# Kernel optimization log

Hardware: AMD Instinct MI355X
Metric: run time of the kernel (lower is better)

The kernel has to match this reference:

```python
import jax, jax.numpy as jnp
import numpy as np

N_HEADS = 16

def _rotate_half(t):
    d = t.shape[-1] // 2
    return jnp.concatenate([-t[..., d:], t[..., :d]], axis=-1)

def _apply_rope(t, cos, sin):
    # t: [B,S,H,dh], cos/sin: [S,1,dh] broadcast over B and H
    return t * cos + _rotate_half(t) * sin

def setup_inputs() -> dict:
    key = jax.random.key(0)
    ks = jax.random.split(key, 7)
    B, S, D = 2, 2048, 2048
    dh = D // N_HEADS
    scale = 1.0 / np.sqrt(D)
    return {
        "x": jax.random.normal(ks[0], (B, S, D), dtype=jnp.float32),
        "rope_cos": jax.random.uniform(ks[1], (S, dh), dtype=jnp.float32),
        "rope_sin": jax.random.uniform(ks[2], (S, dh), dtype=jnp.float32),
        "Wq": jax.random.normal(ks[3], (D, D), dtype=jnp.float32) * scale,
        "Wk": jax.random.normal(ks[4], (D, D), dtype=jnp.float32) * scale,
        "Wv": jax.random.normal(ks[5], (D, D), dtype=jnp.float32) * scale,
        "Wo": jax.random.normal(ks[6], (D, D), dtype=jnp.float32) * scale,
    }

def reference(x, rope_cos, rope_sin, Wq, Wk, Wv, Wo):
    B, S, D = x.shape
    H = N_HEADS
    dh = D // H
    # QKV projections (nn.Linear: x @ W.T), reshape to heads
    q = (x @ Wq.T).reshape(B, S, H, dh)
    k = (x @ Wk.T).reshape(B, S, H, dh)
    v = (x @ Wv.T).reshape(B, S, H, dh)
    cos = rope_cos[:, None, :]  # [S,1,dh]
    sin = rope_sin[:, None, :]
    q = _apply_rope(q, cos, sin)
    k = _apply_rope(k, cos, sin)
    # Attention: [B,H,S,S] scores, scaled softmax
    scores = jnp.einsum("bqhd,bkhd->bhqk", q, k) / jnp.sqrt(jnp.asarray(dh, dtype=x.dtype))
    probs = jax.nn.softmax(scores, axis=-1)
    out = jnp.einsum("bhqk,bkhd->bqhd", probs, v).reshape(B, S, D)
    return out @ Wo.T
```

## Files before the change

kernel.cpp:

```cpp
#include <hip/hip_runtime.h>
#include <hip/hip_bf16.h>

typedef unsigned short u16;
typedef __bf16 bf16x8 __attribute__((ext_vector_type(8)));
typedef float f32x4 __attribute__((ext_vector_type(4)));

__device__ __forceinline__ float bf2f(u16 u) {
  union { unsigned int i; float f; } v; v.i = ((unsigned int)u) << 16; return v.f;
}
__device__ __forceinline__ u16 f2bf(float f) {
  union { float f; unsigned int i; } v; v.f = f;
  unsigned int r = v.i + 0x7fffu + ((v.i >> 16) & 1u);
  return (u16)(r >> 16);
}
__device__ __forceinline__ unsigned cvtpk(float lo, float hi) {
  unsigned r;
  asm("v_cvt_pk_bf16_f32 %0, %1, %2" : "=v"(r) : "v"(lo), "v"(hi));
  return r;
}

__device__ __forceinline__ void async_load16(void* lds, const void* g) {
  __builtin_amdgcn_global_load_lds((const __attribute__((address_space(1))) void*)g,
                                   (__attribute__((address_space(3))) void*)lds, 16, 0, 0);
}

__global__ void convert_all(const float* __restrict__ x, const float* __restrict__ Wq,
                            const float* __restrict__ Wk, const float* __restrict__ Wv,
                            const float* __restrict__ Wo, u16* __restrict__ xb,
                            u16* __restrict__ Wqkb, u16* __restrict__ Wvb,
                            u16* __restrict__ Wob) {
  int bid = blockIdx.x;
  const float* src;
  u16* dst;
  int off;
  if (bid < 8192)       { src = x;  dst = xb;              off = bid; }
  else if (bid < 12288) { src = Wq; dst = Wqkb;            off = bid - 8192; }
  else if (bid < 16384) { src = Wk; dst = Wqkb + 4194304;  off = bid - 12288; }
  else if (bid < 20480) { src = Wv; dst = Wvb;             off = bid - 16384; }
  else                  { src = Wo; dst = Wob;             off = bid - 20480; }
  int i = off * 1024 + threadIdx.x * 4;
  float4 v = *(const float4*)(src + i);
  ushort4 o;
  o.x = f2bf(v.x); o.y = f2bf(v.y); o.z = f2bf(v.z); o.w = f2bf(v.w);
  *(ushort4*)(dst + i) = o;
}

template <int ROPE>
__device__ __forceinline__ void gemm256_body(const u16* __restrict__ A,
                                             const u16* __restrict__ Bm,
                                             u16* __restrict__ C, int M, int N, int K,
                                             int tm, int tn, u16* lds,
                                             const float* __restrict__ cosb,
                                             const float* __restrict__ sinb,
                                             float qscale) {
  const int t = threadIdx.x;
  const int w = t >> 6, l = t & 63;
  const int wm = w >> 2, wn = w & 3;
  const int lr = l & 15, lh = l >> 4;
  const size_t row0 = (size_t)tm * 256, col0 = (size_t)tn * 256;
  const u16* Ag = A + row0 * K;
  const u16* Bg = Bm + col0 * K;

  const int ra = t >> 2, kc = (t & 3) << 3;
  auto stage = [&](int s) {
    u16* dst = lds + (s & 3) * 16384;
    const size_t koff = (size_t)s * 32 + kc;
    async_load16(dst + t * 8,         Ag + (size_t)ra * K + koff);
    async_load16(dst + 4096 + t * 8,  Ag + (size_t)(ra + 128) * K + koff);
    async_load16(dst + 8192 + t * 8,  Bg + (size_t)ra * K + koff);
    async_load16(dst + 12288 + t * 8, Bg + (size_t)(ra + 128) * K + koff);
  };

  f32x4 acc[8][4];
#pragma unroll
  for (int i = 0; i < 8; ++i)
#pragma unroll
    for (int j = 0; j < 4; ++j) acc[i][j] = (f32x4){0.f, 0.f, 0.f, 0.f};

  const int NK = K >> 5;
  stage(0); stage(1); stage(2);

  for (int s = 0; s < NK; ++s) {
    if (s + 2 < NK)      asm volatile("s_waitcnt vmcnt(8)" ::: "memory");
    else if (s + 1 < NK) asm volatile("s_waitcnt vmcnt(4)" ::: "memory");
    else                 asm volatile("s_waitcnt vmcnt(0)" ::: "memory");
    __builtin_amdgcn_s_barrier();
    asm volatile("" ::: "memory");
    if (s + 3 < NK) stage(s + 3);

    const u16* sub = lds + (s & 3) * 16384;
    bf16x8 af[8], bfv[4];
#pragma unroll
    for (int mi = 0; mi < 8; ++mi)
      af[mi] = *reinterpret_cast<const bf16x8*>(sub + (wm * 128 + mi * 16 + lr) * 32 + lh * 8);
#pragma unroll
    for (int ni = 0; ni < 4; ++ni) {
      int colf = ROPE ? ((wn >> 1) * 128 + (wn & 1) * 32 + (ni >> 1) * 64 + (ni & 1) * 16)
                      : (wn * 64 + ni * 16);
      bfv[ni] = *reinterpret_cast<const bf16x8*>(sub + 8192 + (colf + lr) * 32 + lh * 8);
    }
    __builtin_amdgcn_s_setprio(1);
#pragma unroll
    for (int mi = 0; mi < 8; ++mi)
#pragma unroll
      for (int ni = 0; ni < 4; ++ni)
        acc[mi][ni] = __builtin_amdgcn_mfma_f32_16x16x32_bf16(af[mi], bfv[ni], acc[mi][ni], 0, 0, 0);
    __builtin_amdgcn_s_setprio(0);
  }

  if (ROPE) {
    float scale = (2 * tn + (wn >> 1)) < 16 ? qscale : 1.0f;
    size_t colbase = col0 + (wn >> 1) * 128;
#pragma unroll
    for (int mi = 0; mi < 8; ++mi)
#pragma unroll
      for (int r = 0; r < 4; ++r) {
        size_t row = row0 + wm * 128 + mi * 16 + lh * 4 + r;
        int si = (int)(row & 2047);
        const float* cr = cosb + si * 128;
        const float* sr = sinb + si * 128;
#pragma unroll
        for (int ni = 0; ni < 2; ++ni) {
          int dlo = (wn & 1) * 32 + ni * 16 + lr;
          float v0 = acc[mi][ni][r];
          float v1 = acc[mi][ni + 2][r];
          float o0 = (v0 * cr[dlo] - v1 * sr[dlo]) * scale;
          float o1 = (v1 * cr[64 + dlo] + v0 * sr[64 + dlo]) * scale;
          C[row * N + colbase + dlo]      = f2bf(o0);
          C[row * N + colbase + 64 + dlo] = f2bf(o1);
        }
      }
  } else {
#pragma unroll
    for (int mi = 0; mi < 8; ++mi)
#pragma unroll
      for (int ni = 0; ni < 4; ++ni)
#pragma unroll
        for (int r = 0; r < 4; ++r) {
          size_t row = row0 + wm * 128 + mi * 16 + lh * 4 + r;
          size_t col = col0 + wn * 64 + ni * 16 + lr;
          C[row * N + col] = f2bf(acc[mi][ni][r]);
        }
  }
}

__global__ __launch_bounds__(512, 2)
void gemm_qkv256(const u16* __restrict__ xb, const u16* __restrict__ Wqkb,
                 const u16* __restrict__ Wvb, u16* __restrict__ QKb, u16* __restrict__ VTb,
                 const float* __restrict__ cosb, const float* __restrict__ sinb,
                 float qscale) {
  __shared__ __align__(16) u16 lds[4 * 16384];
  int bid = blockIdx.x;
  if (bid < 256) {
    int swz = (bid & 7) * 32 + (bid >> 3);
    gemm256_body<1>(xb, Wqkb, QKb, 4096, 4096, 2048, swz >> 4, swz & 15, lds,
                    cosb, sinb, qscale);
  } else {
    int b2 = bid - 256;
    int swz = (b2 & 7) * 16 + (b2 >> 3);
    gemm256_body<0>(Wvb, xb, VTb, 2048, 4096, 2048, swz >> 4, swz & 15, lds,
                    nullptr, nullptr, 0.f);
  }
}

template <int OUT_F32>
__device__ __forceinline__ void gemm_tile_body(const u16* __restrict__ A,
                                               const u16* __restrict__ Bm,
                                               void* __restrict__ C, int M, int N, int K,
                                               int swz, u16* sA, u16* sB) {
  const int nTn = N >> 7;
  int tm = swz / nTn, tn = swz % nTn;
  const int t = threadIdx.x;
  const int w = t >> 6, l = t & 63;
  const int wr = w >> 1, wc = w & 1;
  const int lr = l & 15, lh = l >> 4;
  const size_t row0 = (size_t)tm * 128, col0 = (size_t)tn * 128;

  f32x4 zero = {0.f, 0.f, 0.f, 0.f};
  f32x4 acc[4][4];
#pragma unroll
  for (int i = 0; i < 4; ++i)
#pragma unroll
    for (int j = 0; j < 4; ++j) acc[i][j] = zero;

  const u16* Ag = A + row0 * K;
  const u16* Bg = Bm + col0 * K;

  for (int k0 = 0; k0 < K; k0 += 32) {
#pragma unroll
    for (int i = 0; i < 2; ++i) {
      int c = i * 256 + t;
      int r = c >> 2, kk = (c & 3) << 3;
      async_load16(sA + (((size_t)i * 256 + w * 64) << 3), Ag + (size_t)r * K + k0 + kk);
      async_load16(sB + (((size_t)i * 256 + w * 64) << 3), Bg + (size_t)r * K + k0 + kk);
    }
    __syncthreads();
    bf16x8 af[4], bfr[4];
#pragma unroll
    for (int mi = 0; mi < 4; ++mi)
      af[mi] = *reinterpret_cast<const bf16x8*>(sA + (wr * 64 + mi * 16 + lr) * 32 + lh * 8);
#pragma unroll
    for (int ni = 0; ni < 4; ++ni)
      bfr[ni] = *reinterpret_cast<const bf16x8*>(sB + (wc * 64 + ni * 16 + lr) * 32 + lh * 8);
#pragma unroll
    for (int mi = 0; mi < 4; ++mi)
#pragma unroll
      for (int ni = 0; ni < 4; ++ni)
        acc[mi][ni] = __builtin_amdgcn_mfma_f32_16x16x32_bf16(af[mi], bfr[ni], acc[mi][ni], 0, 0, 0);
    __syncthreads();
  }

#pragma unroll
  for (int mi = 0; mi < 4; ++mi)
#pragma unroll
    for (int ni = 0; ni < 4; ++ni)
#pragma unroll
      for (int r = 0; r < 4; ++r) {
        size_t row = row0 + wr * 64 + mi * 16 + lh * 4 + r;
        size_t col = col0 + wc * 64 + ni * 16 + lr;
        float v = acc[mi][ni][r];
        if (OUT_F32)
          ((float*)C)[row * N + col] = v;
        else
          ((u16*)C)[row * N + col] = f2bf(v);
      }
}

__global__ __launch_bounds__(256)
void gemm_o(const u16* __restrict__ Ob, const u16* __restrict__ Wob, float* __restrict__ out) {
  __shared__ __align__(16) u16 sA[128 * 32];
  __shared__ __align__(16) u16 sB[128 * 32];
  int bid = blockIdx.x;
  int swz = (bid & 7) * 64 + (bid >> 3);
  gemm_tile_body<1>(Ob, Wob, (void*)out, 4096, 2048, 2048, swz, sA, sB);
}

__global__ __launch_bounds__(256, 2)
void attn_kernel(const u16* __restrict__ QKb, const u16* __restrict__ VT,
                 u16* __restrict__ Ob) {
  __shared__ __align__(16) u16 sK[2][64 * 128];
  __shared__ __align__(16) u16 sV[2][128 * 64];
  __shared__ __align__(16) u16 sP[4][32 * 64];

  int id = blockIdx.x;
  int swz = (id & 7) * 64 + (id >> 3);
  int bh = swz >> 4;
  int qb = swz & 15;
  int b = bh >> 4, h = bh & 15;
  int t = threadIdx.x, w = t >> 6, l = t & 63;
  int lr = l & 15, lh = l >> 4;
  int lr7 = lr & 7;
  int q0 = qb * 128;

  const u16* Kbase = QKb + (size_t)(b * 2048) * 4096 + 2048 + h * 128;
  const u16* Vbase = VT + (size_t)(h * 128) * 4096 + b * 2048;
  u16* sPw = sP[w];

  bf16x8 aq[2][4];
#pragma unroll
  for (int qf = 0; qf < 2; ++qf) {
    size_t qrow = (size_t)(b * 2048 + q0 + w * 32 + qf * 16 + lr) * 4096 + h * 128;
#pragma unroll
    for (int c = 0; c < 4; ++c)
      aq[qf][c] = *reinterpret_cast<const bf16x8*>(QKb + qrow + c * 32 + lh * 8);
  }

  f32x4 zero = {0.f, 0.f, 0.f, 0.f};
  f32x4 acc_o[2][8];
#pragma unroll
  for (int qf = 0; qf < 2; ++qf)
#pragma unroll
    for (int d = 0; d < 8; ++d) acc_o[qf][d] = zero;
  float m_row[2] = {-1e30f, -1e30f};
  float l_row[2] = {0.f, 0.f};

  auto stage = [&](int buf, int kt2) {
    const u16* Kt = Kbase + (size_t)(kt2 * 64) * 4096;
    const u16* Vt = Vbase + kt2 * 64;
#pragma unroll
    for (int it = 0; it < 4; ++it) {
      int o = it * 4096 + t * 16;
      int rowK = o >> 8;
      int cbK = (o & 255) ^ ((rowK & 7) << 4);
      async_load16((u16*)sK[buf] + (o >> 1), Kt + (size_t)rowK * 4096 + (cbK >> 1));
      int rowV = o >> 7;
      int cbV = (o & 127) ^ ((rowV & 7) << 4);
      async_load16((u16*)sV[buf] + (o >> 1), Vt + (size_t)rowV * 4096 + (cbV >> 1));
    }
  };

  stage(0, 0);
  __syncthreads();
  int cur = 0;

  for (int kt = 0; kt < 32; ++kt) {
    if (kt < 31) stage(cur ^ 1, kt + 1);

    const u16* sKc = sK[cur];
    const u16* sVc = sV[cur];

    f32x4 sacc[2][4];
#pragma unroll
    for (int qf = 0; qf < 2; ++qf)
#pragma unroll
      for (int g = 0; g < 4; ++g) sacc[qf][g] = zero;
#pragma unroll
    for (int g = 0; g < 4; ++g) {
      int row = g * 16 + lr;
      int xr = lr7 << 4;
#pragma unroll
      for (int c = 0; c < 4; ++c) {
        int cb = (c * 64 + lh * 16) ^ xr;
        bf16x8 bk = *reinterpret_cast<const bf16x8*>(sKc + row * 128 + (cb >> 1));
        sacc[0][g] = __builtin_amdgcn_mfma_f32_16x16x32_bf16(bk, aq[0][c], sacc[0][g], 0, 0, 0);
        sacc[1][g] = __builtin_amdgcn_mfma_f32_16x16x32_bf16(bk, aq[1][c], sacc[1][g], 0, 0, 0);
      }
    }

#pragma unroll
    for (int qf = 0; qf < 2; ++qf) {
      f32x4 m4;
#pragma unroll
      for (int e = 0; e < 4; ++e)
        m4[e] = fmaxf(fmaxf(sacc[qf][0][e], sacc[qf][1][e]),
                      fmaxf(sacc[qf][2][e], sacc[qf][3][e]));
      float mx = fmaxf(fmaxf(m4[0], m4[1]), fmaxf(m4[2], m4[3]));
      mx = fmaxf(mx, __shfl_xor(mx, 16));
      mx = fmaxf(mx, __shfl_xor(mx, 32));
      float mo = m_row[qf];
      if (!__all(mx <= mo + 8.f)) {
        float mn = fmaxf(mo, mx);
        float al = __builtin_amdgcn_exp2f(mo - mn);
        m_row[qf] = mn;
        l_row[qf] *= al;
#pragma unroll
        for (int d = 0; d < 8; ++d) acc_o[qf][d] *= al;
      }
      float mn = m_row[qf];
#pragma unroll
      for (int g = 0; g < 4; ++g)
#pragma unroll
        for (int e = 0; e < 4; ++e)
          sacc[qf][g][e] = __builtin_amdgcn_exp2f(sacc[qf][g][e] - mn);
      f32x4 s4;
#pragma unroll
      for (int e = 0; e < 4; ++e)
        s4[e] = (sacc[qf][0][e] + sacc[qf][1][e]) + (sacc[qf][2][e] + sacc[qf][3][e]);
      float rs = (s4[0] + s4[1]) + (s4[2] + s4[3]);
      rs += __shfl_xor(rs, 16);
      rs += __shfl_xor(rs, 32);
      l_row[qf] += rs;

      int rowb = (qf * 16 + lr) * 128;
      int xw = lr7 << 4;
#pragma unroll
      for (int g = 0; g < 4; ++g) {
        uint2 pw;
        pw.x = cvtpk(sacc[qf][g][0], sacc[qf][g][1]);
        pw.y = cvtpk(sacc[qf][g][2], sacc[qf][g][3]);
        int cb = (g * 32 + lh * 8) ^ xw;
        *reinterpret_cast<uint2*>(reinterpret_cast<char*>(sPw) + rowb + cb) = pw;
      }
    }

    bf16x8 bp[2][2];
#pragma unroll
    for (int qf = 0; qf < 2; ++qf) {
      int rowb = (qf * 16 + lr) * 128;
      int xr = lr7 << 4;
#pragma unroll
      for (int c2 = 0; c2 < 2; ++c2) {
        int cb = (c2 * 64 + lh * 16) ^ xr;
        bp[qf][c2] = *reinterpret_cast<const bf16x8*>(
            reinterpret_cast<const char*>(sPw) + rowb + cb);
      }
    }
#pragma unroll
    for (int c2 = 0; c2 < 2; ++c2) {
#pragma unroll
      for (int d = 0; d < 8; ++d) {
        int row = d * 16 + lr;
        int cb = (c2 * 64 + lh * 16) ^ (lr7 << 4);
        bf16x8 bv = *reinterpret_cast<const bf16x8*>(sVc + row * 64 + (cb >> 1));
        acc_o[0][d] = __builtin_amdgcn_mfma_f32_16x16x32_bf16(bv, bp[0][c2], acc_o[0][d], 0, 0, 0);
        acc_o[1][d] = __builtin_amdgcn_mfma_f32_16x16x32_bf16(bv, bp[1][c2], acc_o[1][d], 0, 0, 0);
      }
    }

    __syncthreads();
    cur ^= 1;
  }

#pragma unroll
  for (int qf = 0; qf < 2; ++qf) {
    float inv = 1.f / l_row[qf];
    size_t qrow = (size_t)(b * 2048 + q0 + w * 32 + qf * 16 + lr) * 2048 + h * 128;
#pragma unroll
    for (int d = 0; d < 8; ++d) {
      ushort4 o;
      o.x = f2bf(acc_o[qf][d][0] * inv);
      o.y = f2bf(acc_o[qf][d][1] * inv);
      o.z = f2bf(acc_o[qf][d][2] * inv);
      o.w = f2bf(acc_o[qf][d][3] * inv);
      *reinterpret_cast<ushort4*>(Ob + qrow + d * 16 + lh * 4) = o;
    }
  }
}

extern "C" void kernel_launch(void* const* d_in, const int* in_sizes, int n_in,
                              void* d_out, int out_size, void* d_ws, size_t ws_size,
                              hipStream_t stream) {
  const float* x  = (const float*)d_in[0];
  const float* rc = (const float*)d_in[1];
  const float* rs = (const float*)d_in[2];
  const float* Wq = (const float*)d_in[3];
  const float* Wk = (const float*)d_in[4];
  const float* Wv = (const float*)d_in[5];
  const float* Wo = (const float*)d_in[6];
  float* out = (float*)d_out;
  char* ws = (char*)d_ws;
  const size_t MB = 1024 * 1024;
  u16* xb   = (u16*)(ws);
  u16* Wqkb = (u16*)(ws + 16 * MB);
  u16* Wvb  = (u16*)(ws + 32 * MB);
  u16* Wob  = (u16*)(ws + 40 * MB);
  u16* QKb  = (u16*)(ws + 48 * MB);
  u16* VTb  = (u16*)(ws + 80 * MB);
  u16* Ob   = (u16*)(ws + 16 * MB);

  convert_all<<<24576, 256, 0, stream>>>(x, Wq, Wk, Wv, Wo, xb, Wqkb, Wvb, Wob);

  const float qscale = 0.08838834764831845f * 1.4426950408889634f;
  gemm_qkv256<<<384, 512, 0, stream>>>(xb, Wqkb, Wvb, QKb, VTb, rc, rs, qscale);

  attn_kernel<<<512, 256, 0, stream>>>(QKb, VTb, Ob);

  gemm_o<<<512, 256, 0, stream>>>(Ob, Wob, out);
}
```

Measured before the change: 281.8 us.

## Generalize pipelined GEMM body with A-fragment prefetch and reuse for V and O projections

```diff
diff --git a/kernel.cpp b/kernel.cpp
--- a/kernel.cpp
+++ b/kernel.cpp
@@ -45,77 +45,106 @@
   *(ushort4*)(dst + i) = o;
 }
 
-template <int ROPE>
-__device__ __forceinline__ void gemm256_body(const u16* __restrict__ A,
-                                             const u16* __restrict__ Bm,
-                                             u16* __restrict__ C, int M, int N, int K,
-                                             int tm, int tn, u16* lds,
-                                             const float* __restrict__ cosb,
-                                             const float* __restrict__ sinb,
-                                             float qscale) {
+template <int BMHALF, int ROPE, int OUT_F32>
+__device__ __forceinline__ void gemm_pipe_body(const u16* __restrict__ A,
+                                               const u16* __restrict__ Bm,
+                                               void* __restrict__ C, int M, int N, int K,
+                                               int tm, int tn, u16* lds,
+                                               const float* __restrict__ cosb,
+                                               const float* __restrict__ sinb,
+                                               float qscale) {
+  constexpr int MIc = BMHALF / 16;
+  constexpr int SUBU16 = (BMHALF == 128) ? 16384 : 12288;
+  constexpr int BOFF = (BMHALF == 128) ? 8192 : 4096;
   const int t = threadIdx.x;
   const int w = t >> 6, l = t & 63;
   const int wm = w >> 2, wn = w & 3;
   const int lr = l & 15, lh = l >> 4;
-  const size_t row0 = (size_t)tm * 256, col0 = (size_t)tn * 256;
+  const size_t row0 = (size_t)tm * (2 * BMHALF), col0 = (size_t)tn * 256;
   const u16* Ag = A + row0 * K;
   const u16* Bg = Bm + col0 * K;
 
   const int ra = t >> 2, kc = (t & 3) << 3;
   auto stage = [&](int s) {
-    u16* dst = lds + (s & 3) * 16384;
+    u16* dst = lds + (s & 3) * SUBU16;
     const size_t koff = (size_t)s * 32 + kc;
-    async_load16(dst + t * 8,         Ag + (size_t)ra * K + koff);
-    async_load16(dst + 4096 + t * 8,  Ag + (size_t)(ra + 128) * K + koff);
-    async_load16(dst + 8192 + t * 8,  Bg + (size_t)ra * K + koff);
-    async_load16(dst + 12288 + t * 8, Bg + (size_t)(ra + 128) * K + koff);
+    if constexpr (BMHALF == 128) {
+      async_load16(dst + t * 8,         Ag + (size_t)ra * K + koff);
+      async_load16(dst + 4096 + t * 8,  Ag + (size_t)(ra + 128) * K + koff);
+      async_load16(dst + 8192 + t * 8,  Bg + (size_t)ra * K + koff);
+      async_load16(dst + 12288 + t * 8, Bg + (size_t)(ra + 128) * K + koff);
+    } else {
+      async_load16(dst + t * 8,         Ag + (size_t)ra * K + koff);
+      async_load16(dst + 4096 + t * 8,  Bg + (size_t)ra * K + koff);
+      async_load16(dst + 8192 + t * 8,  Bg + (size_t)(ra + 128) * K + koff);
+    }
   };
-
-  f32x4 acc[8][4];
-#pragma unroll
-  for (int i = 0; i < 8; ++i)
+  auto read_af = [&](bf16x8* dst, int s) {
+    const u16* sub = lds + (s & 3) * SUBU16;
+#pragma unroll
+    for (int mi = 0; mi < MIc; ++mi)
+      dst[mi] = *reinterpret_cast<const bf16x8*>(sub + (wm * BMHALF + mi * 16 + lr) * 32 + lh * 8);
+  };
+  auto read_bfv = [&](bf16x8* dst, int s) {
+    const u16* sub = lds + (s & 3) * SUBU16 + BOFF;
+#pragma unroll
+    for (int ni = 0; ni < 4; ++ni) {
+      int colf = ROPE ? ((wn >> 1) * 128 + (wn & 1) * 32 + (ni >> 1) * 64 + (ni & 1) * 16)
+                      : (wn * 64 + ni * 16);
+      dst[ni] = *reinterpret_cast<const bf16x8*>(sub + (colf + lr) * 32 + lh * 8);
+    }
+  };
+
+  f32x4 acc[MIc][4];
+#pragma unroll
+  for (int i = 0; i < MIc; ++i)
 #pragma unroll
     for (int j = 0; j < 4; ++j) acc[i][j] = (f32x4){0.f, 0.f, 0.f, 0.f};
 
   const int NK = K >> 5;
+  bf16x8 afA[MIc], afB[MIc], bfv[4];
+
   stage(0); stage(1); stage(2);
-
-  for (int s = 0; s < NK; ++s) {
-    if (s + 2 < NK)      asm volatile("s_waitcnt vmcnt(8)" ::: "memory");
-    else if (s + 1 < NK) asm volatile("s_waitcnt vmcnt(4)" ::: "memory");
-    else                 asm volatile("s_waitcnt vmcnt(0)" ::: "memory");
+  if constexpr (BMHALF == 128) asm volatile("s_waitcnt vmcnt(8)" ::: "memory");
+  else                         asm volatile("s_waitcnt vmcnt(6)" ::: "memory");
+  __builtin_amdgcn_s_barrier();
+  asm volatile("" ::: "memory");
+  read_af(afA, 0);
+
+  auto pipestep = [&](int s, bf16x8* cur, bf16x8* nxt) {
+    if (s + 2 < NK) {
+      if constexpr (BMHALF == 128) asm volatile("s_waitcnt vmcnt(4)" ::: "memory");
+      else                         asm volatile("s_waitcnt vmcnt(3)" ::: "memory");
+    } else {
+      asm volatile("s_waitcnt vmcnt(0)" ::: "memory");
+    }
     __builtin_amdgcn_s_barrier();
     asm volatile("" ::: "memory");
     if (s + 3 < NK) stage(s + 3);
-
-    const u16* sub = lds + (s & 3) * 16384;
-    bf16x8 af[8], bfv[4];
-#pragma unroll
-    for (int mi = 0; mi < 8; ++mi)
-      af[mi] = *reinterpret_cast<const bf16x8*>(sub + (wm * 128 + mi * 16 + lr) * 32 + lh * 8);
-#pragma unroll
-    for (int ni = 0; ni < 4; ++ni) {
-      int colf = ROPE ? ((wn >> 1) * 128 + (wn & 1) * 32 + (ni >> 1) * 64 + (ni & 1) * 16)
-                      : (wn * 64 + ni * 16);
-      bfv[ni] = *reinterpret_cast<const bf16x8*>(sub + 8192 + (colf + lr) * 32 + lh * 8);
-    }
+    read_bfv(bfv, s);
+    if (s + 1 < NK) read_af(nxt, s + 1);
     __builtin_amdgcn_s_setprio(1);
 #pragma unroll
-    for (int mi = 0; mi < 8; ++mi)
+    for (int mi = 0; mi < MIc; ++mi)
 #pragma unroll
       for (int ni = 0; ni < 4; ++ni)
-        acc[mi][ni] = __builtin_amdgcn_mfma_f32_16x16x32_bf16(af[mi], bfv[ni], acc[mi][ni], 0, 0, 0);
+        acc[mi][ni] = __builtin_amdgcn_mfma_f32_16x16x32_bf16(cur[mi], bfv[ni], acc[mi][ni], 0, 0, 0);
     __builtin_amdgcn_s_setprio(0);
-  }
-
-  if (ROPE) {
+  };
+
+  for (int s = 0; s < NK; s += 2) {
+    pipestep(s, afA, afB);
+    pipestep(s + 1, afB, afA);
+  }
+
+  if constexpr (ROPE) {
     float scale = (2 * tn + (wn >> 1)) < 16 ? qscale : 1.0f;
     size_t colbase = col0 + (wn >> 1) * 128;
 #pragma unroll
-    for (int mi = 0; mi < 8; ++mi)
+    for (int mi = 0; mi < MIc; ++mi)
 #pragma unroll
       for (int r = 0; r < 4; ++r) {
-        size_t row = row0 + wm * 128 + mi * 16 + lh * 4 + r;
+        size_t row = row0 + wm * BMHALF + mi * 16 + lh * 4 + r;
         int si = (int)(row & 2047);
         const float* cr = cosb + si * 128;
         const float* sr = sinb + si * 128;
@@ -126,20 +155,24 @@
           float v1 = acc[mi][ni + 2][r];
           float o0 = (v0 * cr[dlo] - v1 * sr[dlo]) * scale;
           float o1 = (v1 * cr[64 + dlo] + v0 * sr[64 + dlo]) * scale;
-          C[row * N + colbase + dlo]      = f2bf(o0);
-          C[row * N + colbase + 64 + dlo] = f2bf(o1);
+          ((u16*)C)[row * N + colbase + dlo]      = f2bf(o0);
+          ((u16*)C)[row * N + colbase + 64 + dlo] = f2bf(o1);
         }
       }
   } else {
 #pragma unroll
-    for (int mi = 0; mi < 8; ++mi)
+    for (int mi = 0; mi < MIc; ++mi)
 #pragma unroll
       for (int ni = 0; ni < 4; ++ni)
 #pragma unroll
         for (int r = 0; r < 4; ++r) {
-          size_t row = row0 + wm * 128 + mi * 16 + lh * 4 + r;
+          size_t row = row0 + wm * BMHALF + mi * 16 + lh * 4 + r;
           size_t col = col0 + wn * 64 + ni * 16 + lr;
-          C[row * N + col] = f2bf(acc[mi][ni][r]);
+          float v = acc[mi][ni][r];
+          if (OUT_F32)
+            ((float*)C)[row * N + col] = v;
+          else
+            ((u16*)C)[row * N + col] = f2bf(v);
         }
   }
 }
@@ -153,86 +186,23 @@
   int bid = blockIdx.x;
   if (bid < 256) {
     int swz = (bid & 7) * 32 + (bid >> 3);
-    gemm256_body<1>(xb, Wqkb, QKb, 4096, 4096, 2048, swz >> 4, swz & 15, lds,
-                    cosb, sinb, qscale);
+    gemm_pipe_body<128, 1, 0>(xb, Wqkb, QKb, 4096, 4096, 2048, swz >> 4, swz & 15, lds,
+                              cosb, sinb, qscale);
   } else {
     int b2 = bid - 256;
-    int swz = (b2 & 7) * 16 + (b2 >> 3);
-    gemm256_body<0>(Wvb, xb, VTb, 2048, 4096, 2048, swz >> 4, swz & 15, lds,
-                    nullptr, nullptr, 0.f);
-  }
-}
-
-template <int OUT_F32>
-__device__ __forceinline__ void gemm_tile_body(const u16* __restrict__ A,
-                                               const u16* __restrict__ Bm,
-                                               void* __restrict__ C, int M, int N, int K,
-                                               int swz, u16* sA, u16* sB) {
-  const int nTn = N >> 7;
-  int tm = swz / nTn, tn = swz % nTn;
-  const int t = threadIdx.x;
-  const int w = t >> 6, l = t & 63;
-  const int wr = w >> 1, wc = w & 1;
-  const int lr = l & 15, lh = l >> 4;
-  const size_t row0 = (size_t)tm * 128, col0 = (size_t)tn * 128;
-
-  f32x4 zero = {0.f, 0.f, 0.f, 0.f};
-  f32x4 acc[4][4];
-#pragma unroll
-  for (int i = 0; i < 4; ++i)
-#pragma unroll
-    for (int j = 0; j < 4; ++j) acc[i][j] = zero;
-
-  const u16* Ag = A + row0 * K;
-  const u16* Bg = Bm + col0 * K;
-
-  for (int k0 = 0; k0 < K; k0 += 32) {
-#pragma unroll
-    for (int i = 0; i < 2; ++i) {
-      int c = i * 256 + t;
-      int r = c >> 2, kk = (c & 3) << 3;
-      async_load16(sA + (((size_t)i * 256 + w * 64) << 3), Ag + (size_t)r * K + k0 + kk);
-      async_load16(sB + (((size_t)i * 256 + w * 64) << 3), Bg + (size_t)r * K + k0 + kk);
-    }
-    __syncthreads();
-    bf16x8 af[4], bfr[4];
-#pragma unroll
-    for (int mi = 0; mi < 4; ++mi)
-      af[mi] = *reinterpret_cast<const bf16x8*>(sA + (wr * 64 + mi * 16 + lr) * 32 + lh * 8);
-#pragma unroll
-    for (int ni = 0; ni < 4; ++ni)
-      bfr[ni] = *reinterpret_cast<const bf16x8*>(sB + (wc * 64 + ni * 16 + lr) * 32 + lh * 8);
-#pragma unroll
-    for (int mi = 0; mi < 4; ++mi)
-#pragma unroll
-      for (int ni = 0; ni < 4; ++ni)
-        acc[mi][ni] = __builtin_amdgcn_mfma_f32_16x16x32_bf16(af[mi], bfr[ni], acc[mi][ni], 0, 0, 0);
-    __syncthreads();
-  }
-
-#pragma unroll
-  for (int mi = 0; mi < 4; ++mi)
-#pragma unroll
-    for (int ni = 0; ni < 4; ++ni)
-#pragma unroll
-      for (int r = 0; r < 4; ++r) {
-        size_t row = row0 + wr * 64 + mi * 16 + lh * 4 + r;
-        size_t col = col0 + wc * 64 + ni * 16 + lr;
-        float v = acc[mi][ni][r];
-        if (OUT_F32)
-          ((float*)C)[row * N + col] = v;
-        else
-          ((u16*)C)[row * N + col] = f2bf(v);
-      }
-}
-
-__global__ __launch_bounds__(256)
+    int swz = (b2 & 7) * 32 + (b2 >> 3);
+    gemm_pipe_body<64, 0, 0>(Wvb, xb, VTb, 2048, 4096, 2048, swz >> 4, swz & 15, lds,
+                             nullptr, nullptr, 0.f);
+  }
+}
+
+__global__ __launch_bounds__(512, 2)
 void gemm_o(const u16* __restrict__ Ob, const u16* __restrict__ Wob, float* __restrict__ out) {
-  __shared__ __align__(16) u16 sA[128 * 32];
-  __shared__ __align__(16) u16 sB[128 * 32];
+  __shared__ __align__(16) u16 lds[4 * 16384];
   int bid = blockIdx.x;
-  int swz = (bid & 7) * 64 + (bid >> 3);
-  gemm_tile_body<1>(Ob, Wob, (void*)out, 4096, 2048, 2048, swz, sA, sB);
+  int swz = (bid & 7) * 32 + (bid >> 3);
+  gemm_pipe_body<64, 0, 1>(Ob, Wob, (void*)out, 4096, 2048, 2048, swz >> 3, swz & 7, lds,
+                           nullptr, nullptr, 0.f);
 }
 
 __global__ __launch_bounds__(256, 2)
@@ -431,9 +401,9 @@
   convert_all<<<24576, 256, 0, stream>>>(x, Wq, Wk, Wv, Wo, xb, Wqkb, Wvb, Wob);
 
   const float qscale = 0.08838834764831845f * 1.4426950408889634f;
-  gemm_qkv256<<<384, 512, 0, stream>>>(xb, Wqkb, Wvb, QKb, VTb, rc, rs, qscale);
+  gemm_qkv256<<<512, 512, 0, stream>>>(xb, Wqkb, Wvb, QKb, VTb, rc, rs, qscale);
 
   attn_kernel<<<512, 256, 0, stream>>>(QKb, VTb, Ob);
 
-  gemm_o<<<512, 256, 0, stream>>>(Ob, Wob, out);
-}
+  gemm_o<<<256, 512, 0, stream>>>(Ob, Wob, out);
+}
```

Result: faster. 255.0 us (-9.5%).
